# Kernel tuning notes

Measured on AMD Instinct MI355X. Metric: run time of the kernel, lower is better.

Reference implementation:

```python
import jax, jax.numpy as jnp
import numpy as np
from jax import lax

B, N, C_IN, C_OUT = 4, 8192, 64, 128
STRIDE, RADIUS, K, L = 4, 0.1, 32, 2
EPS = 1e-5
M = N // STRIDE


def _bn(x, g, b):
    # training-mode batch norm, channel-first layout (B, C, ...)
    axes = (0,) + tuple(range(2, x.ndim))
    mean = jnp.mean(x, axis=axes, keepdims=True)
    var = jnp.mean((x - mean) ** 2, axis=axes, keepdims=True)
    sh = (1, -1) + (1,) * (x.ndim - 2)
    return (x - mean) * lax.rsqrt(var + EPS) * g.reshape(sh) + b.reshape(sh)


def _fps(points, m):
    # farthest point sampling starting at index 0 (matches fps_cuda semantics)
    b, n, _ = points.shape
    bi = jnp.arange(b)

    def body(carry, _):
        dis, last = carry
        lp = points[bi, last]  # (b,3)
        d = jnp.sum((points - lp[:, None, :]) ** 2, -1)
        dis = jnp.minimum(dis, d)
        return (dis, jnp.argmax(dis, -1).astype(jnp.int32)), last

    init = (jnp.full((b, n), 1e10, points.dtype), jnp.zeros((b,), jnp.int32))
    _, idx = lax.scan(body, init, None, length=m)
    return idx.T  # (b, m)


def _ball_query(radius, k, centroids, points, features):
    # first k points within radius of each centroid; pad with first hit
    b, n, _ = points.shape
    d2 = jnp.sum((centroids[:, :, None, :] - points[:, None, :, :]) ** 2, -1)  # (b,m,n)
    key = jnp.where(d2 < radius * radius, jnp.arange(n, dtype=jnp.int32), n)
    neg, _ = lax.top_k(-key, k)  # k smallest keys = first k in-ball indices
    sel = -neg  # (b,m,k)
    sel = jnp.where(sel == n, sel[..., :1], sel)
    sel = jnp.clip(sel, 0, n - 1)
    bi = jnp.arange(b)[:, None, None]
    gp = jnp.transpose(points[bi, sel], (0, 3, 2, 1))  # (b,3,k,m)
    gf = None
    if features is not None:
        gf = jnp.transpose(features[bi, sel], (0, 3, 2, 1))  # (b,c,k,m)
    return gp, gf


def _forward(pos, x, p):
    b, n, _ = pos.shape
    m = n // STRIDE
    bi = jnp.arange(b)[:, None]
    fps_idx = _fps(pos, m)
    centroids = pos[bi, fps_idx]  # (b,m,3)
    # x_mlp: 1x1 conv + BN + ReLU
    f = jax.nn.relu(_bn(jnp.einsum('bnc,oc->bon', x, p['W_x']), p['g_x'], p['b_x']))
    feats = jnp.transpose(f, (0, 2, 1))  # (b,n,C_OUT)
    gp, gf = _ball_query(RADIUS, K, centroids, pos, feats)
    cT = jnp.transpose(centroids, (0, 2, 1))[:, :, None, :]  # (b,3,1,m)
    gp = (gp - cT) / RADIUS
    gp = jax.nn.relu(_bn(jnp.einsum('bckm,oc->bokm', gp, p['W_ps']), p['g_ps'], p['b_ps']))
    xf = jnp.transpose(jnp.max(gf + gp, axis=2), (0, 2, 1))  # (b,m,C_OUT)
    # gen_pe on downsampled points
    R2 = RADIUS * 2
    gpe, _ = _ball_query(R2, K, centroids, centroids, None)
    gpe = (gpe - cT) / R2
    pe = jax.nn.relu(_bn(jnp.einsum('bckm,oc->bokm', gpe, p['W_pe']), p['g_pe'], p['b_pe']))
    # InvResMLP blocks
    for i in range(L):
        xc = jnp.transpose(xf, (0, 2, 1))  # (b,C,m)
        xc = jax.nn.relu(_bn(jnp.einsum('bcm,oc->bom', xc, p['W1'][i]), p['g1'][i], p['b1'][i]))
        feats_i = jnp.transpose(xc, (0, 2, 1))  # (b,m,C)
        _, gfi = _ball_query(R2, K, centroids, centroids, feats_i)
        g = jnp.max(gfi + pe, axis=2)  # (b,C,m)
        g = jax.nn.relu(_bn(jnp.einsum('bcm,oc->bom', g, p['W2a'][i]), p['g2a'][i], p['b2a'][i]))
        g = _bn(jnp.einsum('bcm,oc->bom', g, p['W2b'][i]), p['g2b'][i], p['b2b'][i])
        xf = jax.nn.relu(feats_i + jnp.transpose(g, (0, 2, 1)))
    return centroids, xf


def setup_inputs() -> dict:
    key = jax.random.key(0)
    ks = jax.random.split(key, 12)
    d = {
        'pos': jax.random.uniform(ks[0], (B, N, 3), jnp.float32),
        'x': jax.random.normal(ks[1], (B, N, C_IN), jnp.float32),
        'W_x': jax.random.normal(ks[2], (C_OUT, C_IN), jnp.float32) * 0.05,
        'g_x': jnp.ones((C_OUT,), jnp.float32), 'b_x': jnp.zeros((C_OUT,), jnp.float32),
        'W_ps': jax.random.normal(ks[3], (C_OUT, 3), jnp.float32) * 0.1,
        'g_ps': jnp.ones((C_OUT,), jnp.float32), 'b_ps': jnp.zeros((C_OUT,), jnp.float32),
        'W_pe': jax.random.normal(ks[4], (C_OUT, 3), jnp.float32) * 0.1,
        'g_pe': jnp.ones((C_OUT,), jnp.float32), 'b_pe': jnp.zeros((C_OUT,), jnp.float32),
        'W1': jax.random.normal(ks[5], (L, C_OUT, C_OUT), jnp.float32) * 0.05,
        'g1': jnp.ones((L, C_OUT), jnp.float32), 'b1': jnp.zeros((L, C_OUT), jnp.float32),
        'W2a': jax.random.normal(ks[6], (L, C_OUT, C_OUT), jnp.float32) * 0.05,
        'g2a': jnp.ones((L, C_OUT), jnp.float32), 'b2a': jnp.zeros((L, C_OUT), jnp.float32),
        'W2b': jax.random.normal(ks[7], (L, C_OUT, C_OUT), jnp.float32) * 0.05,
        'g2b': jnp.ones((L, C_OUT), jnp.float32), 'b2b': jnp.zeros((L, C_OUT), jnp.float32),
    }
    return d


def reference(pos, x, W_x, g_x, b_x, W_ps, g_ps, b_ps, W_pe, g_pe, b_pe,
              W1, g1, b1, W2a, g2a, b2a, W2b, g2b, b2b):
    p = dict(W_x=W_x, g_x=g_x, b_x=b_x, W_ps=W_ps, g_ps=g_ps, b_ps=b_ps,
             W_pe=W_pe, g_pe=g_pe, b_pe=b_pe, W1=W1, g1=g1, b1=b1,
             W2a=W2a, g2a=g2a, b2a=b2a, W2b=W2b, g2b=g2b, b2b=b2b)
    return _forward(pos, x, p)
```

## Files before the change

### kernel.cpp

```cpp
#include <hip/hip_runtime.h>


#define BB 4
#define NN 8192
#define MM 2048
#define KK 32
#define CI 64
#define CO 128
#define SG 16

typedef float vf2 __attribute__((ext_vector_type(2)));

#define ST_X 0
#define MO_PS 256
#define MO_PE 272
#define ST1 288
#define ST2A (288 + 2 * SG * 256)
#define ST2B (ST2A + 2 * SG * 256)
#define ST_TOTAL (ST2B + 512)

__device__ __forceinline__ float sq3(float dx, float dy, float dz) {
#pragma clang fp contract(off)
  return dx * dx + dy * dy + dz * dz;
}

__device__ __forceinline__ void fin_stats_d(const double* st, float gam,
                                            float bet, double cnt, int ch,
                                            float* sc, float* sh) {
  double mean = st[ch] / cnt;
  double var = st[128 + ch] / cnt - mean * mean;
  if (var < 0) var = 0;
  double s = (double)gam / sqrt(var + 1e-5);
  *sc = (float)s;
  *sh = (float)((double)bet - mean * s);
}

__device__ __forceinline__ void fin_grp_d(const double* st, float gam,
                                          float bet, double cnt, int ch,
                                          float* sc, float* sh) {
  double sum = 0, ssq = 0;
#pragma unroll
  for (int g = 0; g < SG; g++) {
    sum += st[g * 256 + ch];
    ssq += st[g * 256 + 128 + ch];
  }
  double mean = sum / cnt;
  double var = ssq / cnt - mean * mean;
  if (var < 0) var = 0;
  double s = (double)gam / sqrt(var + 1e-5);
  *sc = (float)s;
  *sh = (float)((double)bet - mean * s);
}

__device__ __forceinline__ void fin_mom_d(const double* mo, const float* Wrow,
                                          float gam, float bet, double cnt,
                                          float* sc, float* sh) {
  double w0 = Wrow[0], w1 = Wrow[1], w2 = Wrow[2];
  double mx = mo[0] / cnt, my = mo[1] / cnt, mz = mo[2] / cnt;
  double sxx = mo[3] / cnt, sxy = mo[4] / cnt, sxz = mo[5] / cnt;
  double syy = mo[6] / cnt, syz = mo[7] / cnt, szz = mo[8] / cnt;
  double mean = w0 * mx + w1 * my + w2 * mz;
  double ey2 = w0 * w0 * sxx + w1 * w1 * syy + w2 * w2 * szz +
               2.0 * (w0 * w1 * sxy + w0 * w2 * sxz + w1 * w2 * syz);
  double var = ey2 - mean * mean;
  if (var < 0) var = 0;
  double s = (double)gam / sqrt(var + 1e-5);
  *sc = (float)s;
  *sh = (float)((double)bet - mean * s);
}

template <int CTRL>
__device__ __forceinline__ int dpp_i(int v) {
  return __builtin_amdgcn_update_dpp(v, v, CTRL, 0xF, 0xF, false);
}
template <int CTRL>
__device__ __forceinline__ float dpp_f(float v) {
  return __int_as_float(dpp_i<CTRL>(__float_as_int(v)));
}

#define FT 512
#define NP 8
#define NW 8

__global__ __launch_bounds__(FT) void k_fps_conv(
    const float* __restrict__ pos, const float* __restrict__ x,
    const float* __restrict__ W_x, float* __restrict__ cent,
    float* __restrict__ fpre, double* __restrict__ stats) {
  __shared__ alignas(16) unsigned long long s_key[2][NW];
  __shared__ alignas(16) float s_pts[NN * 3];
  __shared__ alignas(16) float s_cent[MM * 3];
  int t = threadIdx.x;
  if (blockIdx.x >= BB) {
    int cb = blockIdx.x - BB;
    int o = t & 127, q = t >> 7;
    float4 w[CI / 4];
    const float4* Wv = (const float4*)(W_x + (size_t)o * CI);
#pragma unroll
    for (int i = 0; i < CI / 4; i++) w[i] = Wv[i];
    int row0 = cb * 128;
    float ssum = 0.f, ssq = 0.f;
    for (int r = 0; r < 128; r += 4) {
      int row = __builtin_amdgcn_readfirstlane(row0 + r + q);
      const float* xr = x + (size_t)row * CI;
      float acc = 0.f;
#pragma unroll
      for (int i = 0; i < CI / 4; i++) {
        float4 a = *(const float4*)(xr + 4 * i);
        acc += a.x * w[i].x + a.y * w[i].y + a.z * w[i].z + a.w * w[i].w;
      }
      fpre[(size_t)row * CO + o] = acc;
      ssum += acc;
      ssq += acc * acc;
    }
    atomicAdd(&stats[ST_X + o], (double)ssum);
    atomicAdd(&stats[ST_X + 128 + o], (double)ssq);
    return;
  }
  int b = blockIdx.x;
  const float* P = pos + (size_t)b * NN * 3;
  float* C = cent + (size_t)b * MM * 3;
  int lane = t & 63, w = t >> 6;
  int ws = __builtin_amdgcn_readfirstlane(w);
  for (int i = t; i < (NN * 3) / 4; i += FT) {
    ((float4*)s_pts)[i] = ((const float4*)P)[i];
  }
  vf2 px[NP], py[NP], pz[NP], ds[NP];
#pragma unroll
  for (int s = 0; s < NP; s++) {
    int ia = (2 * s) * FT + t;
    int ib = ia + FT;
    px[s] = (vf2){P[ia * 3 + 0], P[ib * 3 + 0]};
    py[s] = (vf2){P[ia * 3 + 1], P[ib * 3 + 1]};
    pz[s] = (vf2){P[ia * 3 + 2], P[ib * 3 + 2]};
    ds[s] = (vf2){1e10f, 1e10f};
  }
  float lx = P[0], ly = P[1], lz = P[2];
  if (t == 0) {
    s_cent[0] = lx;
    s_cent[1] = ly;
    s_cent[2] = lz;
  }
  __syncthreads();
  for (int m = 1; m < MM; m++) {
    vf2 l2x = (vf2){lx, lx}, l2y = (vf2){ly, ly}, l2z = (vf2){lz, lz};
    vf2 bmax = (vf2){-1.0f, -1.0f};
    {
#pragma clang fp contract(off)
#pragma unroll
      for (int s = 0; s < NP; s++) {
        vf2 dx = px[s] - l2x;
        vf2 dy = py[s] - l2y;
        vf2 dz = pz[s] - l2z;
        vf2 d2 = dx * dx + dy * dy + dz * dz;
        vf2 nd = __builtin_elementwise_min(ds[s], d2);
        ds[s] = nd;
        bmax = __builtin_elementwise_max(bmax, nd);
      }
    }
    float bv = fmaxf(bmax.x, bmax.y);
    bv = fmaxf(bv, dpp_f<0x111>(bv));
    bv = fmaxf(bv, dpp_f<0x112>(bv));
    bv = fmaxf(bv, dpp_f<0x114>(bv));
    bv = fmaxf(bv, dpp_f<0x118>(bv));
    bv = fmaxf(bv, dpp_f<0x142>(bv));
    bv = fmaxf(bv, dpp_f<0x143>(bv));
    float wmax =
        __int_as_float(__builtin_amdgcn_readlane(__float_as_int(bv), 63));
    unsigned idxw = 0xffffffffu;
#pragma unroll
    for (int s = NP - 1; s >= 0; s--) {
      unsigned long long mby = __ballot(ds[s].y == wmax);
      unsigned basey = (unsigned)((2 * s) * FT + FT + (ws << 6));
      if (mby) idxw = basey + (unsigned)(__ffsll((long long)mby) - 1);
      unsigned long long mbx = __ballot(ds[s].x == wmax);
      unsigned basex = (unsigned)((2 * s) * FT + (ws << 6));
      if (mbx) idxw = basex + (unsigned)(__ffsll((long long)mbx) - 1);
    }
    int pb = m & 1;
    if (lane == 0) {
      s_key[pb][ws] = ((unsigned long long)__float_as_uint(wmax) << 32) |
                      (unsigned long long)(~idxw);
    }
    __syncthreads();
    const ulonglong2* kp = (const ulonglong2*)(&s_key[pb][0]);
    ulonglong2 q0 = kp[0];
    ulonglong2 q1 = kp[1];
    ulonglong2 q2 = kp[2];
    ulonglong2 q3 = kp[3];
    unsigned long long a0 = q0.x > q0.y ? q0.x : q0.y;
    unsigned long long a1 = q1.x > q1.y ? q1.x : q1.y;
    unsigned long long a2 = q2.x > q2.y ? q2.x : q2.y;
    unsigned long long a3 = q3.x > q3.y ? q3.x : q3.y;
    a0 = a0 > a1 ? a0 : a1;
    a2 = a2 > a3 ? a2 : a3;
    unsigned long long kw = a0 > a2 ? a0 : a2;
    unsigned gidx = ~(unsigned)(kw & 0xffffffffull);
    lx = s_pts[gidx * 3 + 0];
    ly = s_pts[gidx * 3 + 1];
    lz = s_pts[gidx * 3 + 2];
    if (t == 0) {
      s_cent[m * 3 + 0] = lx;
      s_cent[m * 3 + 1] = ly;
      s_cent[m * 3 + 2] = lz;
    }
  }
  __syncthreads();
  for (int i = t; i < (MM * 3) / 4; i += FT) {
    ((float4*)C)[i] = ((const float4*)s_cent)[i];
  }
}

__global__ __launch_bounds__(256) void k_bq2(const float* __restrict__ pos,
                                             const float* __restrict__ cent,
                                             int* __restrict__ sel1,
                                             int* __restrict__ sel2,
                                             double* __restrict__ stats) {
  int lane = threadIdx.x & 63, w = threadIdx.x >> 6;
  const float* pts;
  int npts, pair;
  float rsq, inv_r;
  int* sel;
  double* mom;
  int half = (BB * MM) / 4;
  if (blockIdx.x < half) {
    pts = pos; npts = NN; rsq = 0.01f; inv_r = 10.0f;
    sel = sel1; mom = stats + MO_PS;
    pair = blockIdx.x * 4 + w;
  } else {
    pts = cent; npts = MM; rsq = 0.04f; inv_r = 5.0f;
    sel = sel2; mom = stats + MO_PE;
    pair = (blockIdx.x - half) * 4 + w;
  }
  int b = pair / MM;
  const float* P = pts + (size_t)b * npts * 3;
  const float* C = cent + (size_t)pair * 3;
  float cx = C[0], cy = C[1], cz = C[2];
  __shared__ int s_sel[4][KK];
  __shared__ float s_mom[4][9];
  int cnt = 0;
  unsigned long long ltm = (1ull << lane) - 1ull;
  int nit = npts >> 8;
  for (int ch = 0; ch < nit; ch++) {
    int i0 = (ch << 8) + lane;
    bool h0, h1, h2, h3;
    {
      float a0 = P[i0 * 3 + 0], a1 = P[i0 * 3 + 1], a2 = P[i0 * 3 + 2];
      float b0 = P[(i0 + 64) * 3 + 0], b1 = P[(i0 + 64) * 3 + 1],
            b2 = P[(i0 + 64) * 3 + 2];
      float c0 = P[(i0 + 128) * 3 + 0], c1 = P[(i0 + 128) * 3 + 1],
            c2 = P[(i0 + 128) * 3 + 2];
      float e0 = P[(i0 + 192) * 3 + 0], e1 = P[(i0 + 192) * 3 + 1],
            e2 = P[(i0 + 192) * 3 + 2];
      h0 = sq3(a0 - cx, a1 - cy, a2 - cz) < rsq;
      h1 = sq3(b0 - cx, b1 - cy, b2 - cz) < rsq;
      h2 = sq3(c0 - cx, c1 - cy, c2 - cz) < rsq;
      h3 = sq3(e0 - cx, e1 - cy, e2 - cz) < rsq;
    }
    unsigned long long m0 = __ballot(h0);
    unsigned long long m1 = __ballot(h1);
    unsigned long long m2 = __ballot(h2);
    unsigned long long m3 = __ballot(h3);
    if (m0) {
      int k = cnt + __popcll(m0 & ltm);
      if (h0 && k < KK) s_sel[w][k] = i0;
      cnt += __popcll(m0);
    }
    if (m1) {
      int k = cnt + __popcll(m1 & ltm);
      if (h1 && k < KK) s_sel[w][k] = i0 + 64;
      cnt += __popcll(m1);
    }
    if (m2) {
      int k = cnt + __popcll(m2 & ltm);
      if (h2 && k < KK) s_sel[w][k] = i0 + 128;
      cnt += __popcll(m2);
    }
    if (m3) {
      int k = cnt + __popcll(m3 & ltm);
      if (h3 && k < KK) s_sel[w][k] = i0 + 192;
      cnt += __popcll(m3);
    }
    if (cnt >= KK) break;
  }
  int total = cnt < KK ? cnt : KK;
  int myidx = 0;
  if (lane < KK) {
    int v = (lane < total) ? s_sel[w][lane] : s_sel[w][0];
    sel[(size_t)pair * KK + lane] = v;
    myidx = v;
  }
  float gx = 0.f, gy = 0.f, gz = 0.f;
  if (lane < KK) {
    gx = (P[myidx * 3 + 0] - cx) * inv_r;
    gy = (P[myidx * 3 + 1] - cy) * inv_r;
    gz = (P[myidx * 3 + 2] - cz) * inv_r;
  }
  float v9[9] = {gx, gy, gz, gx * gx, gx * gy, gx * gz, gy * gy, gy * gz, gz * gz};
#pragma unroll
  for (int j = 0; j < 9; j++) {
#pragma unroll
    for (int off = 32; off > 0; off >>= 1) v9[j] += __shfl_xor(v9[j], off);
  }
  if (lane == 0) {
#pragma unroll
    for (int j = 0; j < 9; j++) s_mom[w][j] = v9[j];
  }
  __syncthreads();
  if (threadIdx.x < 9) {
    double a = (double)s_mom[0][threadIdx.x] + s_mom[1][threadIdx.x] +
               s_mom[2][threadIdx.x] + s_mom[3][threadIdx.x];
    atomicAdd(&mom[threadIdx.x], a);
  }
}

__global__ __launch_bounds__(128) void k_xf_conv1(
    const float* __restrict__ pos, const float* __restrict__ cent,
    const int* __restrict__ sel1, const float* __restrict__ fpre,
    const float* __restrict__ Wps, const float* __restrict__ g_ps,
    const float* __restrict__ b_ps, const float* __restrict__ g_x,
    const float* __restrict__ b_x, const double* __restrict__ stats,
    const float* __restrict__ W1, float* __restrict__ y1a,
    double* __restrict__ st1out) {
  int pair = blockIdx.x;
  int b = pair >> 11;
  int o = threadIdx.x;
  float sx, hx, sp, hp;
  fin_stats_d(stats + ST_X, g_x[o], b_x[o], (double)(BB * NN), o, &sx, &hx);
  fin_mom_d(stats + MO_PS, Wps + o * 3, g_ps[o], b_ps[o],
            (double)(BB * MM * KK), &sp, &hp);
  float w0 = Wps[o * 3 + 0], w1 = Wps[o * 3 + 1], w2 = Wps[o * 3 + 2];
  const float* C = cent + (size_t)pair * 3;
  float cx = C[0], cy = C[1], cz = C[2];
  const float* P = pos + (size_t)b * NN * 3;
  const float* F = fpre + (size_t)b * NN * CO;
  __shared__ int s_idx[KK];
  __shared__ float s_xf[128];
  if (o < KK) s_idx[o] = sel1[(size_t)pair * KK + o];
  __syncthreads();
  float acc = -1e30f;
#pragma unroll 4
  for (int k = 0; k < KK; k++) {
    int idx = __builtin_amdgcn_readfirstlane(s_idx[k]);
    float gx = (P[idx * 3 + 0] - cx) * 10.0f;
    float gy = (P[idx * 3 + 1] - cy) * 10.0f;
    float gz = (P[idx * 3 + 2] - cz) * 10.0f;
    float y = fmaxf((w0 * gx + w1 * gy + w2 * gz) * sp + hp, 0.f);
    float f = fmaxf(F[(size_t)idx * CO + o] * sx + hx, 0.f);
    float v = y + f;
    acc = v > acc ? v : acc;
  }
  s_xf[o] = acc;
  __syncthreads();
  const float4* Wv = (const float4*)(W1 + (size_t)o * CO);
  const float4* gv = (const float4*)s_xf;
  float dot = 0.f;
#pragma unroll
  for (int i = 0; i < CO / 4; i++) {
    float4 a = gv[i];
    float4 ww = Wv[i];
    dot += a.x * ww.x + a.y * ww.y + a.z * ww.z + a.w * ww.w;
  }
  y1a[(size_t)pair * CO + o] = dot;
  int grp = pair & (SG - 1);
  atomicAdd(&st1out[grp * 256 + o], (double)dot);
  atomicAdd(&st1out[grp * 256 + 128 + o], (double)(dot * dot));
}

__global__ __launch_bounds__(256) void k_conv_bnin(
    const float* __restrict__ in, const float* __restrict__ W,
    const double* __restrict__ st_grp, const float* __restrict__ gam,
    const float* __restrict__ bet, float* __restrict__ out,
    double* __restrict__ stats, int rows_per_block) {
  __shared__ float s_sc[128], s_sh[128];
  int t = threadIdx.x;
  if (t < 128) {
    fin_grp_d(st_grp, gam[t], bet[t], (double)(BB * MM), t, &s_sc[t],
              &s_sh[t]);
  }
  __syncthreads();
  int o = t & 127, half = t >> 7;
  float4 w[CO / 4];
  const float4* Wv = (const float4*)(W + (size_t)o * CO);
#pragma unroll
  for (int i = 0; i < CO / 4; i++) w[i] = Wv[i];
  int row0 = blockIdx.x * rows_per_block;
  float ssum = 0.f, ssq = 0.f;
  for (int r = 0; r < rows_per_block; r += 2) {
    int row = __builtin_amdgcn_readfirstlane(row0 + r + half);
    const float* xr = in + (size_t)row * CO;
    float acc = 0.f;
#pragma unroll
    for (int i = 0; i < CO / 4; i++) {
      float4 a = *(const float4*)(xr + 4 * i);
      a.x = fmaxf(a.x * s_sc[4 * i + 0] + s_sh[4 * i + 0], 0.f);
      a.y = fmaxf(a.y * s_sc[4 * i + 1] + s_sh[4 * i + 1], 0.f);
      a.z = fmaxf(a.z * s_sc[4 * i + 2] + s_sh[4 * i + 2], 0.f);
      a.w = fmaxf(a.w * s_sc[4 * i + 3] + s_sh[4 * i + 3], 0.f);
      acc += a.x * w[i].x + a.y * w[i].y + a.z * w[i].z + a.w * w[i].w;
    }
    out[(size_t)row * CO + o] = acc;
    ssum += acc;
    ssq += acc * acc;
  }
  atomicAdd(&stats[o], (double)ssum);
  atomicAdd(&stats[128 + o], (double)ssq);
}

__global__ __launch_bounds__(256) void k_conv_resid(
    const float* __restrict__ y1prev, const float* __restrict__ y2bprev,
    const double* __restrict__ st1p, const float* __restrict__ g1p,
    const float* __restrict__ b1p, const double* __restrict__ st2bp,
    const float* __restrict__ g2bp, const float* __restrict__ b2bp,
    const float* __restrict__ W, float* __restrict__ y1out,
    double* __restrict__ stats, int rows_per_block) {
  __shared__ float s_s1[128], s_h1[128], s_s2[128], s_h2[128];
  int t = threadIdx.x;
  if (t < 128) {
    fin_grp_d(st1p, g1p[t], b1p[t], (double)(BB * MM), t, &s_s1[t], &s_h1[t]);
    fin_stats_d(st2bp, g2bp[t], b2bp[t], (double)(BB * MM), t, &s_s2[t],
                &s_h2[t]);
  }
  __syncthreads();
  int o = t & 127, half = t >> 7;
  float4 w[CO / 4];
  const float4* Wv = (const float4*)(W + (size_t)o * CO);
#pragma unroll
  for (int i = 0; i < CO / 4; i++) w[i] = Wv[i];
  int row0 = blockIdx.x * rows_per_block;
  float ssum = 0.f, ssq = 0.f;
  for (int r = 0; r < rows_per_block; r += 2) {
    int row = __builtin_amdgcn_readfirstlane(row0 + r + half);
    const float* ar = y1prev + (size_t)row * CO;
    const float* br = y2bprev + (size_t)row * CO;
    float acc = 0.f;
#pragma unroll
    for (int i = 0; i < CO / 4; i++) {
      float4 a = *(const float4*)(ar + 4 * i);
      float4 bb = *(const float4*)(br + 4 * i);
      float x0 = fmaxf(fmaxf(a.x * s_s1[4 * i + 0] + s_h1[4 * i + 0], 0.f) +
                           (bb.x * s_s2[4 * i + 0] + s_h2[4 * i + 0]), 0.f);
      float x1 = fmaxf(fmaxf(a.y * s_s1[4 * i + 1] + s_h1[4 * i + 1], 0.f) +
                           (bb.y * s_s2[4 * i + 1] + s_h2[4 * i + 1]), 0.f);
      float x2 = fmaxf(fmaxf(a.z * s_s1[4 * i + 2] + s_h1[4 * i + 2], 0.f) +
                           (bb.z * s_s2[4 * i + 2] + s_h2[4 * i + 2]), 0.f);
      float x3 = fmaxf(fmaxf(a.w * s_s1[4 * i + 3] + s_h1[4 * i + 3], 0.f) +
                           (bb.w * s_s2[4 * i + 3] + s_h2[4 * i + 3]), 0.f);
      acc += x0 * w[i].x + x1 * w[i].y + x2 * w[i].z + x3 * w[i].w;
    }
    y1out[(size_t)row * CO + o] = acc;
    ssum += acc;
    ssq += acc * acc;
  }
  int grp = blockIdx.x & (SG - 1);
  atomicAdd(&stats[grp * 256 + o], (double)ssum);
  atomicAdd(&stats[grp * 256 + 128 + o], (double)ssq);
}

__global__ __launch_bounds__(128) void k_gconv(
    const float* __restrict__ cent, const int* __restrict__ sel2,
    const float* __restrict__ y1in, const double* __restrict__ st1,
    const float* __restrict__ g1v, const float* __restrict__ b1v,
    const double* __restrict__ mo_pe, const float* __restrict__ Wpe,
    const float* __restrict__ gpe, const float* __restrict__ bpe,
    const float* __restrict__ W2a, float* __restrict__ y2a,
    double* __restrict__ st2a) {
  int pair = blockIdx.x;
  int b = pair >> 11;
  int o = threadIdx.x;
  float s1, h1, se, he;
  fin_grp_d(st1, g1v[o], b1v[o], (double)(BB * MM), o, &s1, &h1);
  fin_mom_d(mo_pe, Wpe + o * 3, gpe[o], bpe[o], (double)(BB * MM * KK), &se,
            &he);
  float w0 = Wpe[o * 3 + 0], w1 = Wpe[o * 3 + 1], w2 = Wpe[o * 3 + 2];
  const float* C = cent + (size_t)pair * 3;
  float cx = C[0], cy = C[1], cz = C[2];
  const float* CB = cent + (size_t)b * MM * 3;
  const float* Y = y1in + (size_t)b * MM * CO;
  __shared__ int s_idx[KK];
  __shared__ float s_g[128];
  if (o < KK) s_idx[o] = sel2[(size_t)pair * KK + o];
  __syncthreads();
  float acc = -1e30f;
#pragma unroll 4
  for (int k = 0; k < KK; k++) {
    int idx = __builtin_amdgcn_readfirstlane(s_idx[k]);
    float gx = (CB[idx * 3 + 0] - cx) * 5.0f;
    float gy = (CB[idx * 3 + 1] - cy) * 5.0f;
    float gz = (CB[idx * 3 + 2] - cz) * 5.0f;
    float pe = fmaxf((w0 * gx + w1 * gy + w2 * gz) * se + he, 0.f);
    float f = fmaxf(Y[(size_t)idx * CO + o] * s1 + h1, 0.f);
    float v = pe + f;
    acc = v > acc ? v : acc;
  }
  s_g[o] = acc;
  __syncthreads();
  const float4* Wv = (const float4*)(W2a + (size_t)o * CO);
  const float4* gv = (const float4*)s_g;
  float dot = 0.f;
#pragma unroll
  for (int i = 0; i < CO / 4; i++) {
    float4 a = gv[i];
    float4 ww = Wv[i];
    dot += a.x * ww.x + a.y * ww.y + a.z * ww.z + a.w * ww.w;
  }
  y2a[(size_t)pair * CO + o] = dot;
  int grp = pair & (SG - 1);
  atomicAdd(&st2a[grp * 256 + o], (double)dot);
  atomicAdd(&st2a[grp * 256 + 128 + o], (double)(dot * dot));
}

__global__ __launch_bounds__(256) void k_resid_fin(
    const float* __restrict__ y1b, const double* __restrict__ st1,
    const float* __restrict__ g1v, const float* __restrict__ b1v,
    const float* __restrict__ y2b, const double* __restrict__ st2b,
    const float* __restrict__ g2bv, const float* __restrict__ b2bv,
    float* __restrict__ xf) {
  int i = blockIdx.x * 256 + threadIdx.x;
  int o = i & 127;
  float s1, h1, s2, h2;
  fin_grp_d(st1, g1v[o], b1v[o], (double)(BB * MM), o, &s1, &h1);
  fin_stats_d(st2b, g2bv[o], b2bv[o], (double)(BB * MM), o, &s2, &h2);
  float f = fmaxf(y1b[i] * s1 + h1, 0.f);
  float v = y2b[i] * s2 + h2;
  xf[i] = fmaxf(f + v, 0.f);
}

extern "C" void kernel_launch(void* const* d_in, const int* in_sizes, int n_in,
                              void* d_out, int out_size, void* d_ws,
                              size_t ws_size, hipStream_t stream) {
  const float* pos = (const float*)d_in[0];
  const float* x = (const float*)d_in[1];
  const float* W_x = (const float*)d_in[2];
  const float* g_x = (const float*)d_in[3];
  const float* b_x = (const float*)d_in[4];
  const float* W_ps = (const float*)d_in[5];
  const float* g_ps = (const float*)d_in[6];
  const float* b_ps = (const float*)d_in[7];
  const float* W_pe = (const float*)d_in[8];
  const float* g_pe = (const float*)d_in[9];
  const float* b_pe = (const float*)d_in[10];
  const float* W1 = (const float*)d_in[11];
  const float* g1 = (const float*)d_in[12];
  const float* b1 = (const float*)d_in[13];
  const float* W2a = (const float*)d_in[14];
  const float* g2a = (const float*)d_in[15];
  const float* b2a = (const float*)d_in[16];
  const float* W2b = (const float*)d_in[17];
  const float* g2b = (const float*)d_in[18];
  const float* b2b = (const float*)d_in[19];

  float* cent = (float*)d_out;
  float* xf = cent + (size_t)BB * MM * 3;

  char* p = (char*)d_ws;
  double* stats = (double*)p; p += (size_t)ST_TOTAL * sizeof(double);
  int* sel1 = (int*)p;        p += (size_t)BB * MM * KK * sizeof(int);
  int* sel2 = (int*)p;        p += (size_t)BB * MM * KK * sizeof(int);
  float* fpre = (float*)p;    p += (size_t)BB * NN * CO * sizeof(float);
  float* y1a = (float*)p;     p += (size_t)BB * MM * CO * sizeof(float);
  float* y1b = (float*)p;     p += (size_t)BB * MM * CO * sizeof(float);
  float* y2a = (float*)p;     p += (size_t)BB * MM * CO * sizeof(float);
  float* y2b = (float*)p;     p += (size_t)BB * MM * CO * sizeof(float);

  hipMemsetAsync(stats, 0, (size_t)ST_TOTAL * sizeof(double), stream);
  k_fps_conv<<<BB + 256, FT, 0, stream>>>(pos, x, W_x, cent, fpre, stats);
  k_bq2<<<(BB * MM) / 2, 256, 0, stream>>>(pos, cent, sel1, sel2, stats);
  k_xf_conv1<<<BB * MM, 128, 0, stream>>>(pos, cent, sel1, fpre, W_ps, g_ps,
                                          b_ps, g_x, b_x, stats, W1, y1a,
                                          stats + ST1);
  k_gconv<<<BB * MM, 128, 0, stream>>>(cent, sel2, y1a, stats + ST1, g1, b1,
                                       stats + MO_PE, W_pe, g_pe, b_pe, W2a,
                                       y2a, stats + ST2A);
  k_conv_bnin<<<128, 256, 0, stream>>>(y2a, W2b, stats + ST2A, g2a, b2a, y2b,
                                       stats + ST2B, 64);
  k_conv_resid<<<128, 256, 0, stream>>>(
      y1a, y2b, stats + ST1, g1, b1, stats + ST2B, g2b, b2b, W1 + CO * CO, y1b,
      stats + ST1 + SG * 256, 64);
  k_gconv<<<BB * MM, 128, 0, stream>>>(cent, sel2, y1b, stats + ST1 + SG * 256,
                                       g1 + 128, b1 + 128, stats + MO_PE, W_pe,
                                       g_pe, b_pe, W2a + CO * CO, y2a,
                                       stats + ST2A + SG * 256);
  k_conv_bnin<<<128, 256, 0, stream>>>(y2a, W2b + CO * CO,
                                       stats + ST2A + SG * 256, g2a + 128,
                                       b2a + 128, y2b, stats + ST2B + 256, 64);
  k_resid_fin<<<(BB * MM * CO) / 256, 256, 0, stream>>>(
      y1b, stats + ST1 + SG * 256, g1 + 128, b1 + 128, y2b,
      stats + ST2B + 256, g2b + 128, b2b + 128, xf);
}
```

Baseline: 2.568 ms.

## Split FPS in halves and overlap first-half ball query with second-half FPS

Farthest point sampling is split across two kernels: the first computes the first half of the centroids and saves its per-point min-distance state to global memory, and the second resumes FPS from that state. Extra blocks in the second kernel run the ball query for the first-half centroids while the four serial FPS blocks keep working, hiding part of the neighbour search behind the latency-bound sequential loop. The remaining ball queries (second-half centroids and the centroid-to-centroid query) run in a follow-up kernel. The cost is an extra launch, a save and restore of the distance state, and co-scheduling the large-LDS FPS blocks with the query blocks.

```diff
diff --git a/kernel.cpp b/kernel.cpp
--- a/kernel.cpp
+++ b/kernel.cpp
@@ -4,6 +4,7 @@
 #define BB 4
 #define NN 8192
 #define MM 2048
+#define HM 1024
 #define KK 32
 #define CI 64
 #define CO 128
@@ -82,10 +83,92 @@
 #define NP 8
 #define NW 8
 
+__device__ __forceinline__ void bq_wave(int pair, const float* __restrict__ pts,
+                                        int npts, float rsq, float inv_r,
+                                        int* __restrict__ sel,
+                                        const float* __restrict__ cent,
+                                        int lane, int* __restrict__ s_selw,
+                                        float* __restrict__ s_momw) {
+  int b = pair >> 11;
+  const float* P = pts + (size_t)b * npts * 3;
+  const float* C = cent + (size_t)pair * 3;
+  float cx = C[0], cy = C[1], cz = C[2];
+  int cnt = 0;
+  unsigned long long ltm = (1ull << lane) - 1ull;
+  int nit = npts >> 8;
+  for (int ch = 0; ch < nit; ch++) {
+    int i0 = (ch << 8) + lane;
+    bool h0, h1, h2, h3;
+    {
+      float a0 = P[i0 * 3 + 0], a1 = P[i0 * 3 + 1], a2 = P[i0 * 3 + 2];
+      float b0 = P[(i0 + 64) * 3 + 0], b1 = P[(i0 + 64) * 3 + 1],
+            b2 = P[(i0 + 64) * 3 + 2];
+      float c0 = P[(i0 + 128) * 3 + 0], c1 = P[(i0 + 128) * 3 + 1],
+            c2 = P[(i0 + 128) * 3 + 2];
+      float e0 = P[(i0 + 192) * 3 + 0], e1 = P[(i0 + 192) * 3 + 1],
+            e2 = P[(i0 + 192) * 3 + 2];
+      h0 = sq3(a0 - cx, a1 - cy, a2 - cz) < rsq;
+      h1 = sq3(b0 - cx, b1 - cy, b2 - cz) < rsq;
+      h2 = sq3(c0 - cx, c1 - cy, c2 - cz) < rsq;
+      h3 = sq3(e0 - cx, e1 - cy, e2 - cz) < rsq;
+    }
+    unsigned long long m0 = __ballot(h0);
+    unsigned long long m1 = __ballot(h1);
+    unsigned long long m2 = __ballot(h2);
+    unsigned long long m3 = __ballot(h3);
+    if (m0) {
+      int k = cnt + __popcll(m0 & ltm);
+      if (h0 && k < KK) s_selw[k] = i0;
+      cnt += __popcll(m0);
+    }
+    if (m1) {
+      int k = cnt + __popcll(m1 & ltm);
+      if (h1 && k < KK) s_selw[k] = i0 + 64;
+      cnt += __popcll(m1);
+    }
+    if (m2) {
+      int k = cnt + __popcll(m2 & ltm);
+      if (h2 && k < KK) s_selw[k] = i0 + 128;
+      cnt += __popcll(m2);
+    }
+    if (m3) {
+      int k = cnt + __popcll(m3 & ltm);
+      if (h3 && k < KK) s_selw[k] = i0 + 192;
+      cnt += __popcll(m3);
+    }
+    if (cnt >= KK) break;
+  }
+  int total = cnt < KK ? cnt : KK;
+  int myidx = 0;
+  if (lane < KK) {
+    int v = (lane < total) ? s_selw[lane] : s_selw[0];
+    sel[(size_t)pair * KK + lane] = v;
+    myidx = v;
+  }
+  float gx = 0.f, gy = 0.f, gz = 0.f;
+  if (lane < KK) {
+    gx = (P[myidx * 3 + 0] - cx) * inv_r;
+    gy = (P[myidx * 3 + 1] - cy) * inv_r;
+    gz = (P[myidx * 3 + 2] - cz) * inv_r;
+  }
+  float v9[9] = {gx, gy, gz, gx * gx, gx * gy, gx * gz, gy * gy, gy * gz,
+                 gz * gz};
+#pragma unroll
+  for (int j = 0; j < 9; j++) {
+#pragma unroll
+    for (int off = 32; off > 0; off >>= 1) v9[j] += __shfl_xor(v9[j], off);
+  }
+  if (lane == 0) {
+#pragma unroll
+    for (int j = 0; j < 9; j++) s_momw[j] = v9[j];
+  }
+}
+
 __global__ __launch_bounds__(FT) void k_fps_conv(
     const float* __restrict__ pos, const float* __restrict__ x,
     const float* __restrict__ W_x, float* __restrict__ cent,
-    float* __restrict__ fpre, double* __restrict__ stats) {
+    float* __restrict__ fpre, double* __restrict__ stats,
+    float* __restrict__ gds) {
   __shared__ alignas(16) unsigned long long s_key[2][NW];
   __shared__ alignas(16) float s_pts[NN * 3];
   __shared__ alignas(16) float s_cent[MM * 3];
@@ -141,7 +224,7 @@
     s_cent[2] = lz;
   }
   __syncthreads();
-  for (int m = 1; m < MM; m++) {
+  for (int m = 1; m < HM; m++) {
     vf2 l2x = (vf2){lx, lx}, l2y = (vf2){ly, ly}, l2z = (vf2){lz, lz};
     vf2 bmax = (vf2){-1.0f, -1.0f};
     {
@@ -205,111 +288,174 @@
     }
   }
   __syncthreads();
-  for (int i = t; i < (MM * 3) / 4; i += FT) {
+  for (int i = t; i < (HM * 3) / 4; i += FT) {
     ((float4*)C)[i] = ((const float4*)s_cent)[i];
   }
-}
-
-__global__ __launch_bounds__(256) void k_bq2(const float* __restrict__ pos,
-                                             const float* __restrict__ cent,
-                                             int* __restrict__ sel1,
-                                             int* __restrict__ sel2,
-                                             double* __restrict__ stats) {
-  int lane = threadIdx.x & 63, w = threadIdx.x >> 6;
+  float2* gd = (float2*)gds + (size_t)b * NP * FT;
+#pragma unroll
+  for (int s = 0; s < NP; s++) {
+    float2 v;
+    v.x = ds[s].x;
+    v.y = ds[s].y;
+    gd[s * FT + t] = v;
+  }
+}
+
+__global__ __launch_bounds__(FT) void k_fps_bq(const float* __restrict__ pos,
+                                               float* __restrict__ cent,
+                                               const float* __restrict__ gds,
+                                               int* __restrict__ sel1,
+                                               double* __restrict__ stats) {
+  __shared__ alignas(16) unsigned long long s_key[2][NW];
+  __shared__ alignas(16) float s_pts[NN * 3];
+  __shared__ alignas(16) float s_cent[MM * 3];
+  __shared__ int s_sel[NW][KK];
+  __shared__ float s_mom[NW][9];
+  int t = threadIdx.x;
+  int lane = t & 63, w = t >> 6;
+  if (blockIdx.x >= BB) {
+    int pi = (blockIdx.x - BB) * 8 + w;
+    int bb = pi >> 10, mi = pi & (HM - 1);
+    int pair = bb * MM + mi;
+    bq_wave(pair, pos, NN, 0.01f, 10.0f, sel1, cent, lane, s_sel[w],
+            s_mom[w]);
+    __syncthreads();
+    if (t < 9) {
+      double a = (double)s_mom[0][t];
+#pragma unroll
+      for (int j = 1; j < NW; j++) a += s_mom[j][t];
+      atomicAdd(&stats[MO_PS + t], a);
+    }
+    return;
+  }
+  int b = blockIdx.x;
+  const float* P = pos + (size_t)b * NN * 3;
+  float* C = cent + (size_t)b * MM * 3;
+  int ws = __builtin_amdgcn_readfirstlane(w);
+  for (int i = t; i < (NN * 3) / 4; i += FT) {
+    ((float4*)s_pts)[i] = ((const float4*)P)[i];
+  }
+  vf2 px[NP], py[NP], pz[NP], ds[NP];
+  const float2* gd = (const float2*)gds + (size_t)b * NP * FT;
+#pragma unroll
+  for (int s = 0; s < NP; s++) {
+    int ia = (2 * s) * FT + t;
+    int ib = ia + FT;
+    px[s] = (vf2){P[ia * 3 + 0], P[ib * 3 + 0]};
+    py[s] = (vf2){P[ia * 3 + 1], P[ib * 3 + 1]};
+    pz[s] = (vf2){P[ia * 3 + 2], P[ib * 3 + 2]};
+    float2 v = gd[s * FT + t];
+    ds[s] = (vf2){v.x, v.y};
+  }
+  float lx = C[(HM - 1) * 3 + 0];
+  float ly = C[(HM - 1) * 3 + 1];
+  float lz = C[(HM - 1) * 3 + 2];
+  __syncthreads();
+  for (int m = HM; m < MM; m++) {
+    vf2 l2x = (vf2){lx, lx}, l2y = (vf2){ly, ly}, l2z = (vf2){lz, lz};
+    vf2 bmax = (vf2){-1.0f, -1.0f};
+    {
+#pragma clang fp contract(off)
+#pragma unroll
+      for (int s = 0; s < NP; s++) {
+        vf2 dx = px[s] - l2x;
+        vf2 dy = py[s] - l2y;
+        vf2 dz = pz[s] - l2z;
+        vf2 d2 = dx * dx + dy * dy + dz * dz;
+        vf2 nd = __builtin_elementwise_min(ds[s], d2);
+        ds[s] = nd;
+        bmax = __builtin_elementwise_max(bmax, nd);
+      }
+    }
+    float bv = fmaxf(bmax.x, bmax.y);
+    bv = fmaxf(bv, dpp_f<0x111>(bv));
+    bv = fmaxf(bv, dpp_f<0x112>(bv));
+    bv = fmaxf(bv, dpp_f<0x114>(bv));
+    bv = fmaxf(bv, dpp_f<0x118>(bv));
+    bv = fmaxf(bv, dpp_f<0x142>(bv));
+    bv = fmaxf(bv, dpp_f<0x143>(bv));
+    float wmax =
+        __int_as_float(__builtin_amdgcn_readlane(__float_as_int(bv), 63));
+    unsigned idxw = 0xffffffffu;
+#pragma unroll
+    for (int s = NP - 1; s >= 0; s--) {
+      unsigned long long mby = __ballot(ds[s].y == wmax);
+      unsigned basey = (unsigned)((2 * s) * FT + FT + (ws << 6));
+      if (mby) idxw = basey + (unsigned)(__ffsll((long long)mby) - 1);
+      unsigned long long mbx = __ballot(ds[s].x == wmax);
+      unsigned basex = (unsigned)((2 * s) * FT + (ws << 6));
+      if (mbx) idxw = basex + (unsigned)(__ffsll((long long)mbx) - 1);
+    }
+    int pb = m & 1;
+    if (lane == 0) {
+      s_key[pb][ws] = ((unsigned long long)__float_as_uint(wmax) << 32) |
+                      (unsigned long long)(~idxw);
+    }
+    __syncthreads();
+    const ulonglong2* kp = (const ulonglong2*)(&s_key[pb][0]);
+    ulonglong2 q0 = kp[0];
+    ulonglong2 q1 = kp[1];
+    ulonglong2 q2 = kp[2];
+    ulonglong2 q3 = kp[3];
+    unsigned long long a0 = q0.x > q0.y ? q0.x : q0.y;
+    unsigned long long a1 = q1.x > q1.y ? q1.x : q1.y;
+    unsigned long long a2 = q2.x > q2.y ? q2.x : q2.y;
+    unsigned long long a3 = q3.x > q3.y ? q3.x : q3.y;
+    a0 = a0 > a1 ? a0 : a1;
+    a2 = a2 > a3 ? a2 : a3;
+    unsigned long long kw = a0 > a2 ? a0 : a2;
+    unsigned gidx = ~(unsigned)(kw & 0xffffffffull);
+    lx = s_pts[gidx * 3 + 0];
+    ly = s_pts[gidx * 3 + 1];
+    lz = s_pts[gidx * 3 + 2];
+    if (t == 0) {
+      s_cent[m * 3 + 0] = lx;
+      s_cent[m * 3 + 1] = ly;
+      s_cent[m * 3 + 2] = lz;
+    }
+  }
+  __syncthreads();
+  for (int i = t + (HM * 3) / 4; i < (MM * 3) / 4; i += FT) {
+    ((float4*)C)[i] = ((const float4*)s_cent)[i];
+  }
+}
+
+__global__ __launch_bounds__(256) void k_bq_rest(const float* __restrict__ pos,
+                                                 const float* __restrict__ cent,
+                                                 int* __restrict__ sel1,
+                                                 int* __restrict__ sel2,
+                                                 double* __restrict__ stats) {
+  __shared__ int s_sel[4][KK];
+  __shared__ float s_mom[4][9];
+  int t = threadIdx.x, lane = t & 63, w = t >> 6;
   const float* pts;
-  int npts, pair;
+  int npts, pair, mo;
   float rsq, inv_r;
   int* sel;
-  double* mom;
-  int half = (BB * MM) / 4;
-  if (blockIdx.x < half) {
-    pts = pos; npts = NN; rsq = 0.01f; inv_r = 10.0f;
-    sel = sel1; mom = stats + MO_PS;
-    pair = blockIdx.x * 4 + w;
+  if (blockIdx.x < (BB * HM) / 4) {
+    int pi = blockIdx.x * 4 + w;
+    int bb = pi >> 10, mi = pi & (HM - 1);
+    pair = bb * MM + HM + mi;
+    pts = pos;
+    npts = NN;
+    rsq = 0.01f;
+    inv_r = 10.0f;
+    sel = sel1;
+    mo = MO_PS;
   } else {
-    pts = cent; npts = MM; rsq = 0.04f; inv_r = 5.0f;
-    sel = sel2; mom = stats + MO_PE;
-    pair = (blockIdx.x - half) * 4 + w;
-  }
-  int b = pair / MM;
-  const float* P = pts + (size_t)b * npts * 3;
-  const float* C = cent + (size_t)pair * 3;
-  float cx = C[0], cy = C[1], cz = C[2];
-  __shared__ int s_sel[4][KK];
-  __shared__ float s_mom[4][9];
-  int cnt = 0;
-  unsigned long long ltm = (1ull << lane) - 1ull;
-  int nit = npts >> 8;
-  for (int ch = 0; ch < nit; ch++) {
-    int i0 = (ch << 8) + lane;
-    bool h0, h1, h2, h3;
-    {
-      float a0 = P[i0 * 3 + 0], a1 = P[i0 * 3 + 1], a2 = P[i0 * 3 + 2];
-      float b0 = P[(i0 + 64) * 3 + 0], b1 = P[(i0 + 64) * 3 + 1],
-            b2 = P[(i0 + 64) * 3 + 2];
-      float c0 = P[(i0 + 128) * 3 + 0], c1 = P[(i0 + 128) * 3 + 1],
-            c2 = P[(i0 + 128) * 3 + 2];
-      float e0 = P[(i0 + 192) * 3 + 0], e1 = P[(i0 + 192) * 3 + 1],
-            e2 = P[(i0 + 192) * 3 + 2];
-      h0 = sq3(a0 - cx, a1 - cy, a2 - cz) < rsq;
-      h1 = sq3(b0 - cx, b1 - cy, b2 - cz) < rsq;
-      h2 = sq3(c0 - cx, c1 - cy, c2 - cz) < rsq;
-      h3 = sq3(e0 - cx, e1 - cy, e2 - cz) < rsq;
-    }
-    unsigned long long m0 = __ballot(h0);
-    unsigned long long m1 = __ballot(h1);
-    unsigned long long m2 = __ballot(h2);
-    unsigned long long m3 = __ballot(h3);
-    if (m0) {
-      int k = cnt + __popcll(m0 & ltm);
-      if (h0 && k < KK) s_sel[w][k] = i0;
-      cnt += __popcll(m0);
-    }
-    if (m1) {
-      int k = cnt + __popcll(m1 & ltm);
-      if (h1 && k < KK) s_sel[w][k] = i0 + 64;
-      cnt += __popcll(m1);
-    }
-    if (m2) {
-      int k = cnt + __popcll(m2 & ltm);
-      if (h2 && k < KK) s_sel[w][k] = i0 + 128;
-      cnt += __popcll(m2);
-    }
-    if (m3) {
-      int k = cnt + __popcll(m3 & ltm);
-      if (h3 && k < KK) s_sel[w][k] = i0 + 192;
-      cnt += __popcll(m3);
-    }
-    if (cnt >= KK) break;
-  }
-  int total = cnt < KK ? cnt : KK;
-  int myidx = 0;
-  if (lane < KK) {
-    int v = (lane < total) ? s_sel[w][lane] : s_sel[w][0];
-    sel[(size_t)pair * KK + lane] = v;
-    myidx = v;
-  }
-  float gx = 0.f, gy = 0.f, gz = 0.f;
-  if (lane < KK) {
-    gx = (P[myidx * 3 + 0] - cx) * inv_r;
-    gy = (P[myidx * 3 + 1] - cy) * inv_r;
-    gz = (P[myidx * 3 + 2] - cz) * inv_r;
-  }
-  float v9[9] = {gx, gy, gz, gx * gx, gx * gy, gx * gz, gy * gy, gy * gz, gz * gz};
-#pragma unroll
-  for (int j = 0; j < 9; j++) {
-#pragma unroll
-    for (int off = 32; off > 0; off >>= 1) v9[j] += __shfl_xor(v9[j], off);
-  }
-  if (lane == 0) {
-#pragma unroll
-    for (int j = 0; j < 9; j++) s_mom[w][j] = v9[j];
-  }
-  __syncthreads();
-  if (threadIdx.x < 9) {
-    double a = (double)s_mom[0][threadIdx.x] + s_mom[1][threadIdx.x] +
-               s_mom[2][threadIdx.x] + s_mom[3][threadIdx.x];
-    atomicAdd(&mom[threadIdx.x], a);
+    pair = (blockIdx.x - (BB * HM) / 4) * 4 + w;
+    pts = cent;
+    npts = MM;
+    rsq = 0.04f;
+    inv_r = 5.0f;
+    sel = sel2;
+    mo = MO_PE;
+  }
+  bq_wave(pair, pts, npts, rsq, inv_r, sel, cent, lane, s_sel[w], s_mom[w]);
+  __syncthreads();
+  if (t < 9) {
+    double a = (double)s_mom[0][t] + s_mom[1][t] + s_mom[2][t] + s_mom[3][t];
+    atomicAdd(&stats[mo + t], a);
   }
 }
 
@@ -561,10 +707,13 @@
   float* y1b = (float*)p;     p += (size_t)BB * MM * CO * sizeof(float);
   float* y2a = (float*)p;     p += (size_t)BB * MM * CO * sizeof(float);
   float* y2b = (float*)p;     p += (size_t)BB * MM * CO * sizeof(float);
+  float* gds = (float*)p;     p += (size_t)BB * NP * FT * 2 * sizeof(float);
 
   hipMemsetAsync(stats, 0, (size_t)ST_TOTAL * sizeof(double), stream);
-  k_fps_conv<<<BB + 256, FT, 0, stream>>>(pos, x, W_x, cent, fpre, stats);
-  k_bq2<<<(BB * MM) / 2, 256, 0, stream>>>(pos, cent, sel1, sel2, stats);
+  k_fps_conv<<<BB + 256, FT, 0, stream>>>(pos, x, W_x, cent, fpre, stats, gds);
+  k_fps_bq<<<BB + (BB * HM) / 8, FT, 0, stream>>>(pos, cent, gds, sel1, stats);
+  k_bq_rest<<<(BB * HM) / 4 + (BB * MM) / 4, 256, 0, stream>>>(pos, cent, sel1,
+                                                               sel2, stats);
   k_xf_conv1<<<BB * MM, 128, 0, stream>>>(pos, cent, sel1, fpre, W_ps, g_ps,
                                           b_ps, g_x, b_x, stats, W1, y1a,
                                           stats + ST1);
```

After: 2.544 ms. About the same (-1.0%).
